# Kernel optimization log

Hardware: AMD Instinct MI355X
Metric: run time of the kernel (lower is better)

Reference implementation:

```python
import jax, jax.numpy as jnp
import numpy as np

K_NEIGH = 20
THRES = 0.5


def setup_inputs() -> dict:
    key = jax.random.key(0)
    # pairwise distance matrix: (batch, num_points, num_points)
    x = jax.random.uniform(key, (16, 4096, 4096), dtype=jnp.float32)
    return {"x": x}


def reference(x):
    # top_k over negated distances == k smallest distances
    vals, nn_idx = jax.lax.top_k(-x, K_NEIGH)          # (B, N, k)
    n = x.shape[1]
    # self index per row, broadcast over k (matches to_add tile in TF code)
    self_idx = jnp.broadcast_to(
        jnp.arange(n, dtype=nn_idx.dtype)[:, None], (n, K_NEIGH)
    )                                                   # (N, k)
    # where distance > thres (i.e. vals < -thres), replace neighbor with self
    mask = vals < -THRES                                # (B, N, k) bool
    nn_idx = jnp.where(mask, self_idx[None, :, :], nn_idx)
    return jax.lax.stop_gradient(nn_idx)
```

## Files before the change

### kernel.cpp

```cpp
#include <hip/hip_runtime.h>
#include <stdint.h>

#define K_NEIGH 20
#define THRES   0.5f
#define NPTS    4096
#define WAVES   4
#define BLOCK   (64 * WAVES)
#define CAP     256
#define TCAND   0.02f

__global__ __launch_bounds__(BLOCK, 4)
void knn_topk_wave(const float* __restrict__ x, int* __restrict__ out) {
    const int wave = threadIdx.x >> 6;
    const int lane = threadIdx.x & 63;
    const int row  = blockIdx.x * WAVES + wave;
    const int self = row & (NPTS - 1);
    const float* __restrict__ xr = x + (size_t)row * NPTS;

    __shared__ unsigned long long keys[WAVES][CAP];
    __shared__ int cnt[WAVES];

    if (lane == 0) cnt[wave] = 0;

    float4 f[16];
#pragma unroll
    for (int m = 0; m < 16; ++m) f[m] = ((const float4*)xr)[lane + 64 * m];

    int local = 0;
#pragma unroll
    for (int m = 0; m < 16; ++m) {
        local += (f[m].x < TCAND) + (f[m].y < TCAND) +
                 (f[m].z < TCAND) + (f[m].w < TCAND);
    }

    int base = 0;
    if (local) base = atomicAdd(&cnt[wave], local);
    if (local && base + local <= CAP) {
        int o = base;
#pragma unroll
        for (int m = 0; m < 16; ++m) {
            const unsigned eb = 4u * ((unsigned)lane + 64u * m);
            const float vv[4] = { f[m].x, f[m].y, f[m].z, f[m].w };
#pragma unroll
            for (int j = 0; j < 4; ++j) {
                if (vv[j] < TCAND) {
                    keys[wave][o++] =
                        ((unsigned long long)__float_as_uint(vv[j]) << 32) | (eb + j);
                }
            }
        }
    }

    const int C = cnt[wave];
    unsigned long long mine = ~0ULL;

    if (C >= K_NEIGH && C <= CAP) {
        unsigned long long s0 = (lane       < C) ? keys[wave][lane      ] : ~0ULL;
        unsigned long long s1 = (lane + 64  < C) ? keys[wave][lane + 64 ] : ~0ULL;
        unsigned long long s2 = (lane + 128 < C) ? keys[wave][lane + 128] : ~0ULL;
        unsigned long long s3 = (lane + 192 < C) ? keys[wave][lane + 192] : ~0ULL;
#pragma unroll
        for (int sel = 0; sel < K_NEIGH; ++sel) {
            unsigned long long a0 = (s0 < s1) ? s0 : s1;
            unsigned long long a1 = (s2 < s3) ? s2 : s3;
            unsigned long long b  = (a0 < a1) ? a0 : a1;
#pragma unroll
            for (int off = 1; off < 64; off <<= 1) {
                unsigned long long o = __shfl_xor(b, off);
                b = (o < b) ? o : b;
            }
            if (s0 == b) s0 = ~0ULL;
            if (s1 == b) s1 = ~0ULL;
            if (s2 == b) s2 = ~0ULL;
            if (s3 == b) s3 = ~0ULL;
            if (lane == sel) mine = b;
        }
    } else {
        unsigned long long prev = 0ULL;
        bool first = true;
        for (int sel = 0; sel < K_NEIGH; ++sel) {
            unsigned long long b = ~0ULL;
#pragma unroll
            for (int m = 0; m < 16; ++m) {
                const unsigned eb = 4u * ((unsigned)lane + 64u * m);
                const float vv[4] = { f[m].x, f[m].y, f[m].z, f[m].w };
#pragma unroll
                for (int j = 0; j < 4; ++j) {
                    unsigned long long kk =
                        ((unsigned long long)__float_as_uint(vv[j]) << 32) | (eb + j);
                    if ((first || kk > prev) && kk < b) b = kk;
                }
            }
            for (int off = 1; off < 64; off <<= 1) {
                unsigned long long o = __shfl_xor(b, off);
                b = (o < b) ? o : b;
            }
            prev = b; first = false;
            if (lane == sel) mine = b;
        }
    }

    if (lane < K_NEIGH) {
        float val = __uint_as_float((unsigned)(mine >> 32));
        int   idx = (int)(mine & 0xFFFFFFFFu);
        out[(size_t)row * K_NEIGH + lane] = (val > THRES) ? self : idx;
    }
}

extern "C" void kernel_launch(void* const* d_in, const int* in_sizes, int n_in,
                              void* d_out, int out_size, void* d_ws, size_t ws_size,
                              hipStream_t stream) {
    const float* x  = (const float*)d_in[0];
    int*        out = (int*)d_out;
    const int n_rows  = in_sizes[0] / NPTS;
    const int n_blocks = n_rows / WAVES;
    knn_topk_wave<<<n_blocks, BLOCK, 0, stream>>>(x, out);
}
```

Before: 1.349 ms.

## Stream row in double-buffered chunks to cut registers and raise occupancy

Instead of holding the entire 4096-element row in 64 registers per lane, the kernel processes it in four 1024-element groups with a double-buffered prefetch of the next group. Candidate compaction into shared memory happens per group. The fallback path now re-reads the row from global memory instead of keeping it in registers. Launch bounds rise from 4 to 6 blocks per CU to use the lower register pressure. The cost is fewer loads in flight per wave, and an extra global re-read on the rare fallback path.

```diff
diff --git a/kernel.cpp b/kernel.cpp
--- a/kernel.cpp
+++ b/kernel.cpp
@@ -9,46 +9,52 @@
 #define CAP     256
 #define TCAND   0.02f
 
-__global__ __launch_bounds__(BLOCK, 4)
-void knn_topk_wave(const float* __restrict__ x, int* __restrict__ out) {
+__global__ __launch_bounds__(BLOCK, 6)
+void knn_topk_stream(const float* __restrict__ x, int* __restrict__ out) {
     const int wave = threadIdx.x >> 6;
     const int lane = threadIdx.x & 63;
     const int row  = blockIdx.x * WAVES + wave;
     const int self = row & (NPTS - 1);
-    const float* __restrict__ xr = x + (size_t)row * NPTS;
+    const float4* __restrict__ xr4 = (const float4*)(x + (size_t)row * NPTS);
 
     __shared__ unsigned long long keys[WAVES][CAP];
     __shared__ int cnt[WAVES];
-
     if (lane == 0) cnt[wave] = 0;
 
-    float4 f[16];
+    float4 bufA[4], bufB[4];
 #pragma unroll
-    for (int m = 0; m < 16; ++m) f[m] = ((const float4*)xr)[lane + 64 * m];
+    for (int m = 0; m < 4; ++m) bufA[m] = xr4[lane + 64 * m];
 
-    int local = 0;
+#pragma unroll 1
+    for (int g = 0; g < 4; ++g) {
+        if (g < 3) {
 #pragma unroll
-    for (int m = 0; m < 16; ++m) {
-        local += (f[m].x < TCAND) + (f[m].y < TCAND) +
-                 (f[m].z < TCAND) + (f[m].w < TCAND);
-    }
-
-    int base = 0;
-    if (local) base = atomicAdd(&cnt[wave], local);
-    if (local && base + local <= CAP) {
-        int o = base;
+            for (int m = 0; m < 4; ++m) bufB[m] = xr4[lane + 64 * (4 * (g + 1) + m)];
+        }
+        int local = 0;
 #pragma unroll
-        for (int m = 0; m < 16; ++m) {
-            const unsigned eb = 4u * ((unsigned)lane + 64u * m);
-            const float vv[4] = { f[m].x, f[m].y, f[m].z, f[m].w };
+        for (int m = 0; m < 4; ++m) {
+            local += (bufA[m].x < TCAND) + (bufA[m].y < TCAND) +
+                     (bufA[m].z < TCAND) + (bufA[m].w < TCAND);
+        }
+        int o = 0;
+        if (local) o = atomicAdd(&cnt[wave], local);
+        if (local && o + local <= CAP) {
 #pragma unroll
-            for (int j = 0; j < 4; ++j) {
-                if (vv[j] < TCAND) {
-                    keys[wave][o++] =
-                        ((unsigned long long)__float_as_uint(vv[j]) << 32) | (eb + j);
+            for (int m = 0; m < 4; ++m) {
+                const unsigned eb = 4u * ((unsigned)lane + 64u * (4 * g + m));
+                const float vv[4] = { bufA[m].x, bufA[m].y, bufA[m].z, bufA[m].w };
+#pragma unroll
+                for (int j = 0; j < 4; ++j) {
+                    if (vv[j] < TCAND) {
+                        keys[wave][o++] =
+                            ((unsigned long long)__float_as_uint(vv[j]) << 32) | (eb + j);
+                    }
                 }
             }
         }
+#pragma unroll
+        for (int m = 0; m < 4; ++m) bufA[m] = bufB[m];
     }
 
     const int C = cnt[wave];
@@ -80,10 +86,10 @@
         bool first = true;
         for (int sel = 0; sel < K_NEIGH; ++sel) {
             unsigned long long b = ~0ULL;
-#pragma unroll
             for (int m = 0; m < 16; ++m) {
+                float4 fv = xr4[lane + 64 * m];
                 const unsigned eb = 4u * ((unsigned)lane + 64u * m);
-                const float vv[4] = { f[m].x, f[m].y, f[m].z, f[m].w };
+                const float vv[4] = { fv.x, fv.y, fv.z, fv.w };
 #pragma unroll
                 for (int j = 0; j < 4; ++j) {
                     unsigned long long kk =
@@ -112,7 +118,7 @@
                               hipStream_t stream) {
     const float* x  = (const float*)d_in[0];
     int*        out = (int*)d_out;
-    const int n_rows  = in_sizes[0] / NPTS;
+    const int n_rows   = in_sizes[0] / NPTS;
     const int n_blocks = n_rows / WAVES;
-    knn_topk_wave<<<n_blocks, BLOCK, 0, stream>>>(x, out);
+    knn_topk_stream<<<n_blocks, BLOCK, 0, stream>>>(x, out);
 }
```

After: 1.344 ms. About the same (-0.4%).
